# Performance work log

Hardware: AMD Instinct MI355X
Metric: run time of the kernel (lower is better)

Reference implementation:

```python
import jax, jax.numpy as jnp
import numpy as np

MASK_FILL = float(-2**32 + 1)


def setup_inputs() -> dict:
    key = jax.random.key(0)
    k1, k2, k3, k4, k5 = jax.random.split(key, 5)
    B, T, D = 64, 1024, 128
    return {
        "key": jax.random.normal(k1, (B, T, D), dtype=jnp.float32),
        "value": jax.random.normal(k2, (B, T, D), dtype=jnp.float32),
        "query": jax.random.normal(k3, (B, T, D), dtype=jnp.float32),
        "mask": jax.random.randint(k4, (B, T, T), 0, 2).astype(jnp.bool_),
        "query_mask": jax.random.uniform(k5, (B, T, 1), dtype=jnp.float32),
        "num_hidden": D,
    }


def reference(key, value, query, mask, query_mask, num_hidden):
    # scores: [B, Tq, Tk]
    scale = 1.0 / jnp.sqrt(jnp.float32(num_hidden))
    attn = jnp.einsum("bqd,bkd->bqk", query, key) * scale
    attn = jnp.where(mask, MASK_FILL, attn)
    attn = jax.nn.softmax(attn, axis=-1)
    attn = attn * query_mask  # broadcast [B, Tq, 1]
    result = jnp.einsum("bqk,bkd->bqd", attn, value)
    return (result, attn)
```

## Files before the change

kernel.cpp:

```cpp
#include <hip/hip_runtime.h>

#define B_   64
#define T_   1024
#define D_   128
#define SCALE_ 0.08838834764831845f
#define FILL_  (-4294967295.0f)
#define OBS  68

typedef __attribute__((ext_vector_type(8))) short short8v;
typedef __attribute__((ext_vector_type(4))) float f32x4;

#define MFMA16(A,Bv,C) __builtin_amdgcn_mfma_f32_16x16x32_bf16((A),(Bv),(C),0,0,0)

__device__ __forceinline__ void split8(const float f[8], short8v& h, short8v& l) {
#pragma unroll
    for (int i = 0; i < 8; ++i) {
        const unsigned int u = __float_as_uint(f[i]);
        h[i] = (short)(u >> 16);
        const float r = f[i] - __uint_as_float(u & 0xffff0000u);
        l[i] = (short)(__float_as_uint(r) >> 16);
    }
}
__device__ __forceinline__ unsigned int packsplit(float f) {
    const unsigned int u = __float_as_uint(f);
    const unsigned int hi = u >> 16;
    const float r = f - __uint_as_float(u & 0xffff0000u);
    const unsigned int lo = __float_as_uint(r) >> 16;
    return hi | (lo << 16);
}

__global__ __launch_bounds__(512)
void mha_kernel(const float* __restrict__ Kp, const float* __restrict__ Vp,
                const float* __restrict__ Qp, const unsigned char* __restrict__ Mp,
                const float* __restrict__ QMp, float* __restrict__ Orp,
                float* __restrict__ Oap)
{
    __shared__ __align__(16) unsigned int Pbuf[8 * 32 * OBS];
    __shared__ float redA[8 * 32];
    __shared__ float redB[8 * 32];

    const int tid  = threadIdx.x;
    const int w    = tid >> 6;
    const int lane = tid & 63;
    const int g    = lane >> 4;
    const int c    = lane & 15;
    const int b    = blockIdx.x >> 5;
    const int q0   = (blockIdx.x & 31) << 5;

    const unsigned int* mw = (const unsigned int*)Mp;
    unsigned int bad = 0u;
#pragma unroll
    for (int i = 0; i < 16; ++i) bad |= (unsigned int)(mw[i] > 1u);
    const bool m32 = (bad == 0u);

    const size_t bt = (size_t)b * T_;

    f32x4 acc[2][8];
#pragma unroll
    for (int mt = 0; mt < 2; ++mt)
#pragma unroll
        for (int nt = 0; nt < 8; ++nt) acc[mt][nt] = (f32x4)0.f;

#pragma unroll
    for (int ks = 0; ks < 4; ++ks) {
        short8v qh[2], ql[2];
#pragma unroll
        for (int mt = 0; mt < 2; ++mt) {
            const float* qp = Qp + (bt + q0 + mt*16 + c) * D_ + ks*32 + g*8;
            float f[8];
#pragma unroll
            for (int i = 0; i < 8; ++i) f[i] = qp[i];
            split8(f, qh[mt], ql[mt]);
        }
#pragma unroll
        for (int nt = 0; nt < 8; ++nt) {
            const float* kp = Kp + (bt + w*128 + nt*16 + c) * D_ + ks*32 + g*8;
            float f[8];
#pragma unroll
            for (int i = 0; i < 8; ++i) f[i] = kp[i];
            short8v kh, kl;
            split8(f, kh, kl);
#pragma unroll
            for (int mt = 0; mt < 2; ++mt) {
                acc[mt][nt] = MFMA16(qh[mt], kh, acc[mt][nt]);
                acc[mt][nt] = MFMA16(qh[mt], kl, acc[mt][nt]);
                acc[mt][nt] = MFMA16(ql[mt], kh, acc[mt][nt]);
            }
        }
    }

    float rmax[2][4];
#pragma unroll
    for (int mt = 0; mt < 2; ++mt)
#pragma unroll
    for (int rg = 0; rg < 4; ++rg) {
        const int row = mt*16 + g*4 + rg;
        const size_t mrow = (bt + q0 + row) * (size_t)T_ + w*128;
        float rm = -3.0e38f;
        if (m32) {
            const int* mi = (const int*)Mp;
#pragma unroll
            for (int nt = 0; nt < 8; ++nt) {
                float s = acc[mt][nt][rg] * SCALE_;
                if (mi[mrow + nt*16 + c]) s = FILL_;
                acc[mt][nt][rg] = s;
                rm = fmaxf(rm, s);
            }
        } else {
#pragma unroll
            for (int nt = 0; nt < 8; ++nt) {
                float s = acc[mt][nt][rg] * SCALE_;
                if (Mp[mrow + nt*16 + c]) s = FILL_;
                acc[mt][nt][rg] = s;
                rm = fmaxf(rm, s);
            }
        }
        rmax[mt][rg] = rm;
    }
#pragma unroll
    for (int mt = 0; mt < 2; ++mt)
#pragma unroll
    for (int rg = 0; rg < 4; ++rg)
#pragma unroll
        for (int off = 1; off < 16; off <<= 1)
            rmax[mt][rg] = fmaxf(rmax[mt][rg], __shfl_xor(rmax[mt][rg], off, 64));
    if (c == 0) {
#pragma unroll
        for (int mt = 0; mt < 2; ++mt)
#pragma unroll
        for (int rg = 0; rg < 4; ++rg)
            redA[w*32 + mt*16 + g*4 + rg] = rmax[mt][rg];
    }
    __syncthreads();
    float rsum[2][4];
#pragma unroll
    for (int mt = 0; mt < 2; ++mt)
#pragma unroll
    for (int rg = 0; rg < 4; ++rg) {
        const int row = mt*16 + g*4 + rg;
        float m = redA[row];
#pragma unroll
        for (int w2 = 1; w2 < 8; ++w2) m = fmaxf(m, redA[w2*32 + row]);
        float s = 0.f;
#pragma unroll
        for (int nt = 0; nt < 8; ++nt) {
            const float e = __expf(acc[mt][nt][rg] - m);
            acc[mt][nt][rg] = e;
            s += e;
        }
#pragma unroll
        for (int off = 1; off < 16; off <<= 1) s += __shfl_xor(s, off, 64);
        rsum[mt][rg] = s;
    }
    if (c == 0) {
#pragma unroll
        for (int mt = 0; mt < 2; ++mt)
#pragma unroll
        for (int rg = 0; rg < 4; ++rg)
            redB[w*32 + mt*16 + g*4 + rg] = rsum[mt][rg];
    }
    __syncthreads();

    unsigned int pk[2][8][4];
#pragma unroll
    for (int mt = 0; mt < 2; ++mt)
#pragma unroll
    for (int rg = 0; rg < 4; ++rg) {
        const int row = mt*16 + g*4 + rg;
        float ssum = redB[row];
#pragma unroll
        for (int w2 = 1; w2 < 8; ++w2) ssum += redB[w2*32 + row];
        const float inv = QMp[bt + q0 + row] / ssum;
        const size_t arow = (bt + q0 + row) * (size_t)T_ + w*128;
#pragma unroll
        for (int nt = 0; nt < 8; ++nt) {
            const float p = acc[mt][nt][rg] * inv;
            Oap[arow + nt*16 + c] = p;
            pk[mt][nt][rg] = packsplit(p);
        }
    }

    f32x4 o[2][8];
#pragma unroll
    for (int mt = 0; mt < 2; ++mt)
#pragma unroll
        for (int nt = 0; nt < 8; ++nt) o[mt][nt] = (f32x4)0.f;

#pragma unroll
    for (int chunk = 0; chunk < 2; ++chunk) {
        __syncthreads();
        if ((w >> 2) == chunk) {
#pragma unroll
            for (int mt = 0; mt < 2; ++mt)
#pragma unroll
            for (int nt = 0; nt < 8; ++nt)
#pragma unroll
            for (int rg = 0; rg < 4; ++rg) {
                const int kl  = (w & 3)*128 + nt*16 + c;
                const int row = mt*16 + g*4 + rg;
                Pbuf[kl*33 + row] = pk[mt][nt][rg];
            }
        }
        __syncthreads();
#pragma unroll
        for (int ks2 = 0; ks2 < 2; ++ks2) {
            const int klb = w*64 + ks2*32;
            short8v ph[2], pl[2];
#pragma unroll
            for (int mt = 0; mt < 2; ++mt) {
                const int base = (klb + g*8)*33 + mt*16 + c;
#pragma unroll
                for (int i = 0; i < 8; ++i) {
                    const unsigned int x = Pbuf[base + i*33];
                    ph[mt][i] = (short)(x & 0xffffu);
                    pl[mt][i] = (short)(x >> 16);
                }
            }
#pragma unroll
            for (int nt = 0; nt < 8; ++nt) {
                const float* vp = Vp + (bt + chunk*512 + klb + g*8) * D_ + nt*16 + c;
                float f[8];
#pragma unroll
                for (int i = 0; i < 8; ++i) f[i] = vp[(size_t)i * D_];
                short8v vh, vl;
                split8(f, vh, vl);
#pragma unroll
                for (int mt = 0; mt < 2; ++mt) {
                    o[mt][nt] = MFMA16(ph[mt], vh, o[mt][nt]);
                    o[mt][nt] = MFMA16(ph[mt], vl, o[mt][nt]);
                    o[mt][nt] = MFMA16(pl[mt], vh, o[mt][nt]);
                }
            }
        }
    }

    float* Ob = (float*)Pbuf;
#pragma unroll
    for (int half = 0; half < 2; ++half) {
        __syncthreads();
#pragma unroll
        for (int mt = 0; mt < 2; ++mt)
#pragma unroll
        for (int nq = 0; nq < 4; ++nq) {
            const int nt = half*4 + nq;
#pragma unroll
            for (int rg = 0; rg < 4; ++rg) {
                const int row = mt*16 + g*4 + rg;
                Ob[(w*32 + row)*OBS + nq*16 + c] = o[mt][nt][rg];
            }
        }
        __syncthreads();
        {
            const int row = tid >> 4;
            const int d0  = (tid & 15) << 2;
            float s0 = 0.f, s1 = 0.f, s2 = 0.f, s3 = 0.f;
#pragma unroll
            for (int w2 = 0; w2 < 8; ++w2) {
                const float* p = &Ob[(w2*32 + row)*OBS + d0];
                s0 += p[0]; s1 += p[1]; s2 += p[2]; s3 += p[3];
            }
            float4 r; r.x = s0; r.y = s1; r.z = s2; r.w = s3;
            *(float4*)&Orp[(bt + q0 + row) * D_ + half*64 + d0] = r;
        }
    }
}

extern "C" void kernel_launch(void* const* d_in, const int* in_sizes, int n_in,
                              void* d_out, int out_size, void* d_ws, size_t ws_size,
                              hipStream_t stream)
{
    const float* Kp  = (const float*)d_in[0];
    const float* Vp  = (const float*)d_in[1];
    const float* Qp  = (const float*)d_in[2];
    const unsigned char* Mp = (const unsigned char*)d_in[3];
    const float* QMp = (const float*)d_in[4];
    float* Orp = (float*)d_out;
    float* Oap = Orp + (size_t)B_ * T_ * D_;

    hipLaunchKernelGGL(mha_kernel, dim3(B_ * 32), dim3(512), 0, stream,
                       Kp, Vp, Qp, Mp, QMp, Orp, Oap);
}
```

Measured before the change: 794.4 us.

## Restructure PV stage to split output columns across waves with LDS-staged V

The P·V stage is reorganized so each wave owns 16 output columns across the full key range, instead of a 64-key slice of all 128 columns. This removes the cross-wave LDS reduction of partial outputs. V tiles of 64 rows are staged cooperatively into swizzled LDS with float4 loads, and P is written one 64-key chunk at a time into a small buffer. The change also adds a min-blocks launch bound and remaps block IDs to interleave batches across XCDs. The cost is 16 iterations each with two barriers, and waves sit idle during P writes.

After: 861.4 us. 1.08x slower.

```diff
diff --git a/kernel.cpp b/kernel.cpp
--- a/kernel.cpp
+++ b/kernel.cpp
@@ -5,7 +5,7 @@
 #define D_   128
 #define SCALE_ 0.08838834764831845f
 #define FILL_  (-4294967295.0f)
-#define OBS  68
+#define VST  132
 
 typedef __attribute__((ext_vector_type(8))) short short8v;
 typedef __attribute__((ext_vector_type(4))) float f32x4;
@@ -29,13 +29,14 @@
     return hi | (lo << 16);
 }
 
-__global__ __launch_bounds__(512)
+__global__ __launch_bounds__(512, 4)
 void mha_kernel(const float* __restrict__ Kp, const float* __restrict__ Vp,
                 const float* __restrict__ Qp, const unsigned char* __restrict__ Mp,
                 const float* __restrict__ QMp, float* __restrict__ Orp,
                 float* __restrict__ Oap)
 {
-    __shared__ __align__(16) unsigned int Pbuf[8 * 32 * OBS];
+    __shared__ __align__(16) float Vlds[64 * VST];
+    __shared__ unsigned int Pc[64 * 33];
     __shared__ float redA[8 * 32];
     __shared__ float redB[8 * 32];
 
@@ -44,8 +45,9 @@
     const int lane = tid & 63;
     const int g    = lane >> 4;
     const int c    = lane & 15;
-    const int b    = blockIdx.x >> 5;
-    const int q0   = (blockIdx.x & 31) << 5;
+    const int wg   = (blockIdx.x & 7) * 256 + (blockIdx.x >> 3);
+    const int b    = wg >> 5;
+    const int q0   = (wg & 31) << 5;
 
     const unsigned int* mw = (const unsigned int*)Mp;
     unsigned int bad = 0u;
@@ -180,89 +182,74 @@
         }
     }
 
-    f32x4 o[2][8];
-#pragma unroll
-    for (int mt = 0; mt < 2; ++mt)
-#pragma unroll
-        for (int nt = 0; nt < 8; ++nt) o[mt][nt] = (f32x4)0.f;
-
-#pragma unroll
-    for (int chunk = 0; chunk < 2; ++chunk) {
+    f32x4 o[2];
+    o[0] = (f32x4)0.f;
+    o[1] = (f32x4)0.f;
+
+    const int vrow = tid >> 3;
+    const int vcg  = tid & 7;
+
+#define WRITE_P(NB)                                                        \
+    {                                                                      \
+        _Pragma("unroll")                                                  \
+        for (int mt = 0; mt < 2; ++mt)                                     \
+        _Pragma("unroll")                                                  \
+        for (int n4 = 0; n4 < 4; ++n4)                                     \
+        _Pragma("unroll")                                                  \
+        for (int rg = 0; rg < 4; ++rg)                                     \
+            Pc[(n4*16 + c)*33 + mt*16 + g*4 + rg] = pk[mt][(NB) + n4][rg]; \
+    }
+
+    for (int kc = 0; kc < 16; ++kc) {
         __syncthreads();
-        if ((w >> 2) == chunk) {
-#pragma unroll
-            for (int mt = 0; mt < 2; ++mt)
-#pragma unroll
-            for (int nt = 0; nt < 8; ++nt)
-#pragma unroll
-            for (int rg = 0; rg < 4; ++rg) {
-                const int kl  = (w & 3)*128 + nt*16 + c;
-                const int row = mt*16 + g*4 + rg;
-                Pbuf[kl*33 + row] = pk[mt][nt][rg];
-            }
+        if (w == (kc >> 1)) {
+            if (kc & 1) { WRITE_P(4) } else { WRITE_P(0) }
+        }
+        {
+            const float* vp = Vp + (bt + kc*64 + vrow) * D_ + vcg*16;
+            float* dst = &Vlds[vrow * VST + ((vcg ^ ((vrow >> 3) & 3)) << 4)];
+#pragma unroll
+            for (int j = 0; j < 4; ++j)
+                *(float4*)&dst[j*4] = *(const float4*)&vp[j*4];
         }
         __syncthreads();
 #pragma unroll
         for (int ks2 = 0; ks2 < 2; ++ks2) {
-            const int klb = w*64 + ks2*32;
             short8v ph[2], pl[2];
 #pragma unroll
             for (int mt = 0; mt < 2; ++mt) {
-                const int base = (klb + g*8)*33 + mt*16 + c;
+                const int base = (ks2*32 + g*8)*33 + mt*16 + c;
 #pragma unroll
                 for (int i = 0; i < 8; ++i) {
-                    const unsigned int x = Pbuf[base + i*33];
+                    const unsigned int x = Pc[base + i*33];
                     ph[mt][i] = (short)(x & 0xffffu);
                     pl[mt][i] = (short)(x >> 16);
                 }
             }
-#pragma unroll
-            for (int nt = 0; nt < 8; ++nt) {
-                const float* vp = Vp + (bt + chunk*512 + klb + g*8) * D_ + nt*16 + c;
-                float f[8];
-#pragma unroll
-                for (int i = 0; i < 8; ++i) f[i] = vp[(size_t)i * D_];
-                short8v vh, vl;
-                split8(f, vh, vl);
-#pragma unroll
-                for (int mt = 0; mt < 2; ++mt) {
-                    o[mt][nt] = MFMA16(ph[mt], vh, o[mt][nt]);
-                    o[mt][nt] = MFMA16(ph[mt], vl, o[mt][nt]);
-                    o[mt][nt] = MFMA16(pl[mt], vh, o[mt][nt]);
-                }
-            }
-        }
-    }
-
-    float* Ob = (float*)Pbuf;
-#pragma unroll
-    for (int half = 0; half < 2; ++half) {
-        __syncthreads();
-#pragma unroll
-        for (int mt = 0; mt < 2; ++mt)
-#pragma unroll
-        for (int nq = 0; nq < 4; ++nq) {
-            const int nt = half*4 + nq;
-#pragma unroll
-            for (int rg = 0; rg < 4; ++rg) {
-                const int row = mt*16 + g*4 + rg;
-                Ob[(w*32 + row)*OBS + nq*16 + c] = o[mt][nt][rg];
-            }
-        }
-        __syncthreads();
-        {
-            const int row = tid >> 4;
-            const int d0  = (tid & 15) << 2;
-            float s0 = 0.f, s1 = 0.f, s2 = 0.f, s3 = 0.f;
-#pragma unroll
-            for (int w2 = 0; w2 < 8; ++w2) {
-                const float* p = &Ob[(w2*32 + row)*OBS + d0];
-                s0 += p[0]; s1 += p[1]; s2 += p[2]; s3 += p[3];
-            }
-            float4 r; r.x = s0; r.y = s1; r.z = s2; r.w = s3;
-            *(float4*)&Orp[(bt + q0 + row) * D_ + half*64 + d0] = r;
-        }
-    }
+            float fv[8];
+            {
+                const int kb   = ks2*32 + g*8;
+                const int dsw  = (w*16 + c) ^ ((((kb) >> 3) & 3) << 4);
+                const int base = kb * VST + dsw;
+#pragma unroll
+                for (int i = 0; i < 8; ++i) fv[i] = Vlds[base + i * VST];
+            }
+            short8v vh, vl;
+            split8(fv, vh, vl);
+#pragma unroll
+            for (int mt = 0; mt < 2; ++mt) {
+                o[mt] = MFMA16(ph[mt], vh, o[mt]);
+                o[mt] = MFMA16(ph[mt], vl, o[mt]);
+                o[mt] = MFMA16(pl[mt], vh, o[mt]);
+            }
+        }
+    }
+
+#pragma unroll
+    for (int mt = 0; mt < 2; ++mt)
+#pragma unroll
+    for (int rg = 0; rg < 4; ++rg)
+        Orp[(bt + q0 + mt*16 + g*4 + rg) * D_ + w*16 + c] = o[mt][rg];
 }
 
 extern "C" void kernel_launch(void* const* d_in, const int* in_sizes, int n_in,
```
